# Kernel optimization log

Hardware: AMD Instinct MI355X
Metric: run time of the kernel (lower is better)

Reference implementation:

```python
import jax, jax.numpy as jnp
import numpy as np

N_NODES = 50000
N_EDGES = 800000
IN_DIM = 128
OUT_DIM = 128


def setup_inputs() -> dict:
    key = jax.random.key(0)
    k1, k2, k3, k4, k5 = jax.random.split(key, 5)
    x = jax.random.normal(k1, (N_NODES, IN_DIM), dtype=jnp.float32)
    # Xavier-uniform-ish scale for the two weight matrices
    scale = float(np.sqrt(6.0 / (IN_DIM + OUT_DIM)))
    Wg = jax.random.uniform(k2, (OUT_DIM, IN_DIM), dtype=jnp.float32, minval=-scale, maxval=scale)
    Wl = jax.random.uniform(k3, (OUT_DIM, IN_DIM), dtype=jnp.float32, minval=-scale, maxval=scale)
    bias = jnp.zeros((OUT_DIM,), dtype=jnp.float32)
    neigh_idx = jax.random.randint(k4, (N_EDGES,), 0, N_NODES, dtype=jnp.int32)
    seg_ids = jnp.sort(jax.random.randint(k5, (N_EDGES,), 0, N_NODES, dtype=jnp.int32))
    return {"x": x, "Wg": Wg, "Wl": Wl, "bias": bias,
            "neigh_idx": neigh_idx, "seg_ids": seg_ids}


def reference(x, Wg, Wl, bias, neigh_idx, seg_ids):
    N = x.shape[0]
    # global 1x1 map on all nodes (self path)
    global_maps = x @ Wg.T                                  # [N, out]
    # per-edge neighbor features: local + global maps of the neighbor
    neigh_x = x[neigh_idx]                                  # [E, in]
    mixed = neigh_x @ Wl.T + global_maps[neigh_idx]         # [E, out]
    # segment-mean over each destination node's neighbors
    sums = jax.ops.segment_sum(mixed, seg_ids, num_segments=N)            # [N, out]
    cnt = jax.ops.segment_sum(jnp.ones((seg_ids.shape[0],), x.dtype), seg_ids, num_segments=N)  # [N]
    mean = sums / jnp.maximum(cnt, 1.0)[:, None]
    # deg == 0 nodes: neigh_agg falls back to global_maps (as in the torch loop)
    neigh_agg = jnp.where((cnt > 0)[:, None], mean, global_maps)
    out = neigh_agg + global_maps + bias
    return jax.nn.elu(out)
```

## Files before the change

### kernel.cpp

```cpp
#include <hip/hip_runtime.h>
#include <hip/hip_bf16.h>

#define NN 50000
#define NE 800000
#define DIM 128
#define NTILES (NN / 16)
#define GEMM_BLOCKS 784

#define XB_BLOCKS 3125
#define OFF_BLOCKS 196
#define V_BLOCKS 128

typedef float f32x4 __attribute__((ext_vector_type(4)));
typedef __bf16 bf16x8 __attribute__((ext_vector_type(8)));

static __device__ __forceinline__ float bflo(unsigned v) {
    unsigned b = v << 16; return __builtin_bit_cast(float, b);
}
static __device__ __forceinline__ float bfhi(unsigned v) {
    unsigned b = v & 0xffff0000u; return __builtin_bit_cast(float, b);
}
static __device__ __forceinline__ unsigned short bfbits(float f) {
    __bf16 b = (__bf16)f; return __builtin_bit_cast(unsigned short, b);
}

__global__ void __launch_bounds__(256) prep(const float* __restrict__ x,
        const float* __restrict__ Wg, const float* __restrict__ Wl,
        const int* __restrict__ seg,
        __bf16* __restrict__ xb, int* __restrict__ off, __bf16* __restrict__ V) {
    int b = blockIdx.x;
    int t = threadIdx.x;
    if (b < XB_BLOCKS) {
        int i = b * 256 + t;
        const float* p = x + (size_t)i * 8;
        f32x4 v0 = *reinterpret_cast<const f32x4*>(p);
        f32x4 v1 = *reinterpret_cast<const f32x4*>(p + 4);
        bf16x8 o;
        o[0]=(__bf16)v0[0]; o[1]=(__bf16)v0[1]; o[2]=(__bf16)v0[2]; o[3]=(__bf16)v0[3];
        o[4]=(__bf16)v1[0]; o[5]=(__bf16)v1[1]; o[6]=(__bf16)v1[2]; o[7]=(__bf16)v1[3];
        *reinterpret_cast<bf16x8*>(xb + (size_t)i * 8) = o;
    } else if (b < XB_BLOCKS + OFF_BLOCKS) {
        int n = (b - XB_BLOCKS) * 256 + t;
        if (n <= NN) {
            int lo = 0, hi = NE;
            while (lo < hi) {
                int mid = (lo + hi) >> 1;
                if (seg[mid] < n) lo = mid + 1; else hi = mid;
            }
            off[n] = lo;
        }
    } else {
        int i = (b - XB_BLOCKS - OFF_BLOCKS) * 256 + t;
        int d = i >> 8;
        int k = i & 255;
        float v;
        if (k < DIM) v = Wg[d * DIM + k];
        else         v = Wg[d * DIM + (k - DIM)] + Wl[d * DIM + (k - DIM)];
        V[i] = (__bf16)v;
    }
}

__global__ void __launch_bounds__(256) seg_mean(const __bf16* __restrict__ xb,
        const int* __restrict__ nidx, const int* __restrict__ off,
        int* __restrict__ cnt_ws, __bf16* __restrict__ meanb) {
    int n = blockIdx.x * 4 + (threadIdx.x >> 6);
    if (n >= NN) return;
    int lane = threadIdx.x & 63;
    int s = off[n], e = off[n + 1];
    const unsigned* xu = reinterpret_cast<const unsigned*>(xb);
    float a0 = 0.f, a1 = 0.f, b0 = 0.f, b1 = 0.f;
    int i = s;
    for (; i + 8 <= e; i += 8) {
        unsigned v0 = xu[nidx[i]   * 64 + lane];
        unsigned v1 = xu[nidx[i+1] * 64 + lane];
        unsigned v2 = xu[nidx[i+2] * 64 + lane];
        unsigned v3 = xu[nidx[i+3] * 64 + lane];
        unsigned v4 = xu[nidx[i+4] * 64 + lane];
        unsigned v5 = xu[nidx[i+5] * 64 + lane];
        unsigned v6 = xu[nidx[i+6] * 64 + lane];
        unsigned v7 = xu[nidx[i+7] * 64 + lane];
        a0 += bflo(v0) + bflo(v2); a1 += bfhi(v0) + bfhi(v2);
        b0 += bflo(v1) + bflo(v3); b1 += bfhi(v1) + bfhi(v3);
        a0 += bflo(v4) + bflo(v6); a1 += bfhi(v4) + bfhi(v6);
        b0 += bflo(v5) + bflo(v7); b1 += bfhi(v5) + bfhi(v7);
    }
    for (; i + 4 <= e; i += 4) {
        unsigned v0 = xu[nidx[i]   * 64 + lane];
        unsigned v1 = xu[nidx[i+1] * 64 + lane];
        unsigned v2 = xu[nidx[i+2] * 64 + lane];
        unsigned v3 = xu[nidx[i+3] * 64 + lane];
        a0 += bflo(v0) + bflo(v2); a1 += bfhi(v0) + bfhi(v2);
        b0 += bflo(v1) + bflo(v3); b1 += bfhi(v1) + bfhi(v3);
    }
    for (; i < e; ++i) {
        unsigned v = xu[nidx[i] * 64 + lane];
        a0 += bflo(v); a1 += bfhi(v);
    }
    float s0 = a0 + b0, s1 = a1 + b1;
    int c = e - s;
    float inv = c > 0 ? 1.f / (float)c : 0.f;
    unsigned o = (unsigned)bfbits(s0 * inv) | ((unsigned)bfbits(s1 * inv) << 16);
    reinterpret_cast<unsigned*>(meanb)[n * 64 + lane] = o;
    if (lane == 0) cnt_ws[n] = c;
}

__global__ void __launch_bounds__(256) gemm_ep(const __bf16* __restrict__ xb,
        const __bf16* __restrict__ meanb, const __bf16* __restrict__ V,
        const float* __restrict__ bias, const int* __restrict__ cnt_ws,
        float* __restrict__ out) {
    int tid = threadIdx.x;
    int w = tid >> 6;
    int lane = tid & 63;
    int rowin = lane & 15;
    int kg = lane >> 4;
    int rbase = kg * 4;

    bf16x8 Bf[8][2];
    #pragma unroll
    for (int s = 0; s < 8; ++s)
        #pragma unroll
        for (int ff = 0; ff < 2; ++ff) {
            int d = (w * 2 + ff) * 16 + rowin;
            Bf[s][ff] = *reinterpret_cast<const bf16x8*>(&V[d * 256 + s * 32 + kg * 8]);
        }
    float bs0 = bias[(w * 2) * 16 + rowin];
    float bs1 = bias[(w * 2 + 1) * 16 + rowin];

    for (int t = blockIdx.x; t < NTILES; t += gridDim.x) {
        int m0 = t * 16;
        int row = m0 + rowin;
        f32x4 acc0 = {}, acc1 = {};
        #pragma unroll
        for (int s = 0; s < 4; ++s) {
            bf16x8 a = *reinterpret_cast<const bf16x8*>(&xb[row * DIM + s * 32 + kg * 8]);
            acc0 = __builtin_amdgcn_mfma_f32_16x16x32_bf16(a, Bf[s][0], acc0, 0, 0, 0);
            acc1 = __builtin_amdgcn_mfma_f32_16x16x32_bf16(a, Bf[s][1], acc1, 0, 0, 0);
        }
        #pragma unroll
        for (int s = 0; s < 4; ++s) {
            bf16x8 a = *reinterpret_cast<const bf16x8*>(&meanb[row * DIM + s * 32 + kg * 8]);
            acc0 = __builtin_amdgcn_mfma_f32_16x16x32_bf16(a, Bf[s + 4][0], acc0, 0, 0, 0);
            acc1 = __builtin_amdgcn_mfma_f32_16x16x32_bf16(a, Bf[s + 4][1], acc1, 0, 0, 0);
        }
        #pragma unroll
        for (int r = 0; r < 4; ++r) {
            int n = m0 + rbase + r;
            int c = cnt_ws[n];
            float v0 = acc0[r];
            float z0 = v0 + (c == 0 ? v0 : 0.f) + bs0;
            out[n * DIM + (w * 2) * 16 + rowin] = z0 > 0.f ? z0 : expm1f(z0);
            float v1 = acc1[r];
            float z1 = v1 + (c == 0 ? v1 : 0.f) + bs1;
            out[n * DIM + (w * 2 + 1) * 16 + rowin] = z1 > 0.f ? z1 : expm1f(z1);
        }
    }
}

extern "C" void kernel_launch(void* const* d_in, const int* in_sizes, int n_in,
                              void* d_out, int out_size, void* d_ws, size_t ws_size,
                              hipStream_t stream) {
    const float* x    = (const float*)d_in[0];
    const float* Wg   = (const float*)d_in[1];
    const float* Wl   = (const float*)d_in[2];
    const float* bias = (const float*)d_in[3];
    const int*   nidx = (const int*)d_in[4];
    const int*   seg  = (const int*)d_in[5];
    float* out = (float*)d_out;

    char* p = (char*)d_ws;
    __bf16* V = (__bf16*)p;       p += DIM * 256 * 2;
    int* off = (int*)p;           p += (((NN + 1) * 4) + 511) & ~511ull;
    int* cnt = (int*)p;           p += ((NN * 4) + 511) & ~511ull;
    __bf16* meanb = (__bf16*)p;   p += (size_t)NN * DIM * 2;
    __bf16* xb = (__bf16*)p;

    prep     <<<XB_BLOCKS + OFF_BLOCKS + V_BLOCKS, 256, 0, stream>>>(x, Wg, Wl, seg, xb, off, V);
    seg_mean <<<(NN + 3) / 4, 256, 0, stream>>>(xb, nidx, off, cnt, meanb);
    gemm_ep  <<<GEMM_BLOCKS, 256, 0, stream>>>(xb, meanb, V, bias, cnt, out);
}
```

Before: 146.0 us.

## Store gathered node features as fp8 and read fp32 x directly in GEMM

```diff
diff --git a/kernel.cpp b/kernel.cpp
--- a/kernel.cpp
+++ b/kernel.cpp
@@ -7,19 +7,15 @@
 #define NTILES (NN / 16)
 #define GEMM_BLOCKS 784
 
-#define XB_BLOCKS 3125
+#define XF8_BLOCKS 3125
 #define OFF_BLOCKS 196
 #define V_BLOCKS 128
 
 typedef float f32x4 __attribute__((ext_vector_type(4)));
+typedef float f32x2 __attribute__((ext_vector_type(2)));
+typedef int   i32x2 __attribute__((ext_vector_type(2)));
 typedef __bf16 bf16x8 __attribute__((ext_vector_type(8)));
 
-static __device__ __forceinline__ float bflo(unsigned v) {
-    unsigned b = v << 16; return __builtin_bit_cast(float, b);
-}
-static __device__ __forceinline__ float bfhi(unsigned v) {
-    unsigned b = v & 0xffff0000u; return __builtin_bit_cast(float, b);
-}
 static __device__ __forceinline__ unsigned short bfbits(float f) {
     __bf16 b = (__bf16)f; return __builtin_bit_cast(unsigned short, b);
 }
@@ -27,20 +23,23 @@
 __global__ void __launch_bounds__(256) prep(const float* __restrict__ x,
         const float* __restrict__ Wg, const float* __restrict__ Wl,
         const int* __restrict__ seg,
-        __bf16* __restrict__ xb, int* __restrict__ off, __bf16* __restrict__ V) {
+        unsigned char* __restrict__ xf8, int* __restrict__ off,
+        __bf16* __restrict__ V) {
     int b = blockIdx.x;
     int t = threadIdx.x;
-    if (b < XB_BLOCKS) {
+    if (b < XF8_BLOCKS) {
         int i = b * 256 + t;
         const float* p = x + (size_t)i * 8;
         f32x4 v0 = *reinterpret_cast<const f32x4*>(p);
         f32x4 v1 = *reinterpret_cast<const f32x4*>(p + 4);
-        bf16x8 o;
-        o[0]=(__bf16)v0[0]; o[1]=(__bf16)v0[1]; o[2]=(__bf16)v0[2]; o[3]=(__bf16)v0[3];
-        o[4]=(__bf16)v1[0]; o[5]=(__bf16)v1[1]; o[6]=(__bf16)v1[2]; o[7]=(__bf16)v1[3];
-        *reinterpret_cast<bf16x8*>(xb + (size_t)i * 8) = o;
-    } else if (b < XB_BLOCKS + OFF_BLOCKS) {
-        int n = (b - XB_BLOCKS) * 256 + t;
+        int lo = __builtin_amdgcn_cvt_pk_fp8_f32(v0[0], v0[1], 0, false);
+        lo     = __builtin_amdgcn_cvt_pk_fp8_f32(v0[2], v0[3], lo, true);
+        int hi = __builtin_amdgcn_cvt_pk_fp8_f32(v1[0], v1[1], 0, false);
+        hi     = __builtin_amdgcn_cvt_pk_fp8_f32(v1[2], v1[3], hi, true);
+        i32x2 o = {lo, hi};
+        *reinterpret_cast<i32x2*>(xf8 + (size_t)i * 8) = o;
+    } else if (b < XF8_BLOCKS + OFF_BLOCKS) {
+        int n = (b - XF8_BLOCKS) * 256 + t;
         if (n <= NN) {
             int lo = 0, hi = NE;
             while (lo < hi) {
@@ -50,7 +49,7 @@
             off[n] = lo;
         }
     } else {
-        int i = (b - XB_BLOCKS - OFF_BLOCKS) * 256 + t;
+        int i = (b - XF8_BLOCKS - OFF_BLOCKS) * 256 + t;
         int d = i >> 8;
         int k = i & 255;
         float v;
@@ -60,41 +59,54 @@
     }
 }
 
-__global__ void __launch_bounds__(256) seg_mean(const __bf16* __restrict__ xb,
+__global__ void __launch_bounds__(256) seg_mean(const unsigned char* __restrict__ xf8,
         const int* __restrict__ nidx, const int* __restrict__ off,
         int* __restrict__ cnt_ws, __bf16* __restrict__ meanb) {
     int n = blockIdx.x * 4 + (threadIdx.x >> 6);
     if (n >= NN) return;
     int lane = threadIdx.x & 63;
     int s = off[n], e = off[n + 1];
-    const unsigned* xu = reinterpret_cast<const unsigned*>(xb);
+    const unsigned short* xu = reinterpret_cast<const unsigned short*>(xf8);
     float a0 = 0.f, a1 = 0.f, b0 = 0.f, b1 = 0.f;
     int i = s;
     for (; i + 8 <= e; i += 8) {
-        unsigned v0 = xu[nidx[i]   * 64 + lane];
-        unsigned v1 = xu[nidx[i+1] * 64 + lane];
-        unsigned v2 = xu[nidx[i+2] * 64 + lane];
-        unsigned v3 = xu[nidx[i+3] * 64 + lane];
-        unsigned v4 = xu[nidx[i+4] * 64 + lane];
-        unsigned v5 = xu[nidx[i+5] * 64 + lane];
-        unsigned v6 = xu[nidx[i+6] * 64 + lane];
-        unsigned v7 = xu[nidx[i+7] * 64 + lane];
-        a0 += bflo(v0) + bflo(v2); a1 += bfhi(v0) + bfhi(v2);
-        b0 += bflo(v1) + bflo(v3); b1 += bfhi(v1) + bfhi(v3);
-        a0 += bflo(v4) + bflo(v6); a1 += bfhi(v4) + bfhi(v6);
-        b0 += bflo(v5) + bflo(v7); b1 += bfhi(v5) + bfhi(v7);
+        unsigned short u0 = xu[nidx[i]   * 64 + lane];
+        unsigned short u1 = xu[nidx[i+1] * 64 + lane];
+        unsigned short u2 = xu[nidx[i+2] * 64 + lane];
+        unsigned short u3 = xu[nidx[i+3] * 64 + lane];
+        unsigned short u4 = xu[nidx[i+4] * 64 + lane];
+        unsigned short u5 = xu[nidx[i+5] * 64 + lane];
+        unsigned short u6 = xu[nidx[i+6] * 64 + lane];
+        unsigned short u7 = xu[nidx[i+7] * 64 + lane];
+        f32x2 f0 = __builtin_amdgcn_cvt_pk_f32_fp8((int)u0, false);
+        f32x2 f1 = __builtin_amdgcn_cvt_pk_f32_fp8((int)u1, false);
+        f32x2 f2 = __builtin_amdgcn_cvt_pk_f32_fp8((int)u2, false);
+        f32x2 f3 = __builtin_amdgcn_cvt_pk_f32_fp8((int)u3, false);
+        f32x2 f4 = __builtin_amdgcn_cvt_pk_f32_fp8((int)u4, false);
+        f32x2 f5 = __builtin_amdgcn_cvt_pk_f32_fp8((int)u5, false);
+        f32x2 f6 = __builtin_amdgcn_cvt_pk_f32_fp8((int)u6, false);
+        f32x2 f7 = __builtin_amdgcn_cvt_pk_f32_fp8((int)u7, false);
+        a0 += f0[0] + f2[0]; a1 += f0[1] + f2[1];
+        b0 += f1[0] + f3[0]; b1 += f1[1] + f3[1];
+        a0 += f4[0] + f6[0]; a1 += f4[1] + f6[1];
+        b0 += f5[0] + f7[0]; b1 += f5[1] + f7[1];
     }
     for (; i + 4 <= e; i += 4) {
-        unsigned v0 = xu[nidx[i]   * 64 + lane];
-        unsigned v1 = xu[nidx[i+1] * 64 + lane];
-        unsigned v2 = xu[nidx[i+2] * 64 + lane];
-        unsigned v3 = xu[nidx[i+3] * 64 + lane];
-        a0 += bflo(v0) + bflo(v2); a1 += bfhi(v0) + bfhi(v2);
-        b0 += bflo(v1) + bflo(v3); b1 += bfhi(v1) + bfhi(v3);
+        unsigned short u0 = xu[nidx[i]   * 64 + lane];
+        unsigned short u1 = xu[nidx[i+1] * 64 + lane];
+        unsigned short u2 = xu[nidx[i+2] * 64 + lane];
+        unsigned short u3 = xu[nidx[i+3] * 64 + lane];
+        f32x2 f0 = __builtin_amdgcn_cvt_pk_f32_fp8((int)u0, false);
+        f32x2 f1 = __builtin_amdgcn_cvt_pk_f32_fp8((int)u1, false);
+        f32x2 f2 = __builtin_amdgcn_cvt_pk_f32_fp8((int)u2, false);
+        f32x2 f3 = __builtin_amdgcn_cvt_pk_f32_fp8((int)u3, false);
+        a0 += f0[0] + f2[0]; a1 += f0[1] + f2[1];
+        b0 += f1[0] + f3[0]; b1 += f1[1] + f3[1];
     }
     for (; i < e; ++i) {
-        unsigned v = xu[nidx[i] * 64 + lane];
-        a0 += bflo(v); a1 += bfhi(v);
+        unsigned short u = xu[nidx[i] * 64 + lane];
+        f32x2 f = __builtin_amdgcn_cvt_pk_f32_fp8((int)u, false);
+        a0 += f[0]; a1 += f[1];
     }
     float s0 = a0 + b0, s1 = a1 + b1;
     int c = e - s;
@@ -104,7 +116,7 @@
     if (lane == 0) cnt_ws[n] = c;
 }
 
-__global__ void __launch_bounds__(256) gemm_ep(const __bf16* __restrict__ xb,
+__global__ void __launch_bounds__(256) gemm_ep(const float* __restrict__ x,
         const __bf16* __restrict__ meanb, const __bf16* __restrict__ V,
         const float* __restrict__ bias, const int* __restrict__ cnt_ws,
         float* __restrict__ out) {
@@ -132,7 +144,12 @@
         f32x4 acc0 = {}, acc1 = {};
         #pragma unroll
         for (int s = 0; s < 4; ++s) {
-            bf16x8 a = *reinterpret_cast<const bf16x8*>(&xb[row * DIM + s * 32 + kg * 8]);
+            const float* xp = x + (size_t)row * DIM + s * 32 + kg * 8;
+            f32x4 v0 = *reinterpret_cast<const f32x4*>(xp);
+            f32x4 v1 = *reinterpret_cast<const f32x4*>(xp + 4);
+            bf16x8 a;
+            a[0]=(__bf16)v0[0]; a[1]=(__bf16)v0[1]; a[2]=(__bf16)v0[2]; a[3]=(__bf16)v0[3];
+            a[4]=(__bf16)v1[0]; a[5]=(__bf16)v1[1]; a[6]=(__bf16)v1[2]; a[7]=(__bf16)v1[3];
             acc0 = __builtin_amdgcn_mfma_f32_16x16x32_bf16(a, Bf[s][0], acc0, 0, 0, 0);
             acc1 = __builtin_amdgcn_mfma_f32_16x16x32_bf16(a, Bf[s][1], acc1, 0, 0, 0);
         }
@@ -168,13 +185,13 @@
     float* out = (float*)d_out;
 
     char* p = (char*)d_ws;
-    __bf16* V = (__bf16*)p;       p += DIM * 256 * 2;
-    int* off = (int*)p;           p += (((NN + 1) * 4) + 511) & ~511ull;
-    int* cnt = (int*)p;           p += ((NN * 4) + 511) & ~511ull;
-    __bf16* meanb = (__bf16*)p;   p += (size_t)NN * DIM * 2;
-    __bf16* xb = (__bf16*)p;
+    __bf16* V = (__bf16*)p;           p += DIM * 256 * 2;
+    int* off = (int*)p;               p += (((NN + 1) * 4) + 511) & ~511ull;
+    int* cnt = (int*)p;               p += ((NN * 4) + 511) & ~511ull;
+    __bf16* meanb = (__bf16*)p;       p += (size_t)NN * DIM * 2;
+    unsigned char* xf8 = (unsigned char*)p;
 
-    prep     <<<XB_BLOCKS + OFF_BLOCKS + V_BLOCKS, 256, 0, stream>>>(x, Wg, Wl, seg, xb, off, V);
-    seg_mean <<<(NN + 3) / 4, 256, 0, stream>>>(xb, nidx, off, cnt, meanb);
-    gemm_ep  <<<GEMM_BLOCKS, 256, 0, stream>>>(xb, meanb, V, bias, cnt, out);
+    prep     <<<XF8_BLOCKS + OFF_BLOCKS + V_BLOCKS, 256, 0, stream>>>(x, Wg, Wl, seg, xf8, off, V);
+    seg_mean <<<(NN + 3) / 4, 256, 0, stream>>>(xf8, nidx, off, cnt, meanb);
+    gemm_ep  <<<GEMM_BLOCKS, 256, 0, stream>>>(x, meanb, V, bias, cnt, out);
 }
```

After: 150.4 us. +3.0%, slower.
